# Kernel optimization log

Measured on AMD Instinct MI355X. Metric: run time of the kernel, lower is better.

Reference implementation:

```python
import jax, jax.numpy as jnp
import numpy as np

B, D_TCF, T, GAF_DIM, DK, HIDDEN, N_CLASSES = 128, 512, 1024, 256, 32, 64, 4
EPS = 1e-5

def _glorot(key, shape):
    fan_out, fan_in = shape
    lim = float(np.sqrt(6.0 / (fan_in + fan_out)))
    return jax.random.uniform(key, shape, jnp.float32, -lim, lim)

def setup_inputs() -> dict:
    key = jax.random.key(0)
    ks = jax.random.split(key, 8)
    return {
        "tcf_feat": jax.random.normal(ks[0], (B, D_TCF, T), jnp.float32),
        "gaf_emb": jax.random.normal(ks[1], (B, GAF_DIM), jnp.float32),
        "Wq": _glorot(ks[2], (DK, D_TCF)),        # q_proj.weight [out,in]
        "Wkv": _glorot(ks[3], (DK, GAF_DIM)),     # kv_proj.weight
        "Wout": _glorot(ks[4], (D_TCF, DK)),      # out_proj.weight
        "ln1_g": jnp.ones((D_TCF,), jnp.float32),
        "ln1_b": jnp.zeros((D_TCF,), jnp.float32),
        "W1": _glorot(ks[5], (HIDDEN, D_TCF)),
        "b1": jnp.zeros((HIDDEN,), jnp.float32),
        "ln2_g": jnp.ones((HIDDEN,), jnp.float32),
        "ln2_b": jnp.zeros((HIDDEN,), jnp.float32),
        "W2": _glorot(ks[6], (N_CLASSES, HIDDEN)),
        "b2": jnp.zeros((N_CLASSES,), jnp.float32),
    }

def _layernorm(x, g, b):
    mu = jnp.mean(x, axis=-1, keepdims=True)
    var = jnp.mean(jnp.square(x - mu), axis=-1, keepdims=True)
    return (x - mu) * jax.lax.rsqrt(var + EPS) * g + b

def reference(tcf_feat, gaf_emb, Wq, Wkv, Wout, ln1_g, ln1_b, W1, b1, ln2_g, ln2_b, W2, b2):
    scale = DK ** (-0.5)
    x = jnp.swapaxes(tcf_feat, 1, 2)                      # [B,T,d_tcf]
    Q = jnp.einsum('btd,kd->btk', x, Wq)                  # [B,T,dk]
    KV = gaf_emb @ Wkv.T                                  # [B,dk] (single key/value)
    scores = jnp.einsum('btk,bk->bt', Q, KV) * scale      # [B,T]
    w = jax.nn.softmax(scores, axis=1)                    # softmax over T (dim=1)
    attn_out = w[:, :, None] * KV[:, None, :]             # [B,T,dk]
    y = _layernorm(x + jnp.einsum('btk,dk->btd', attn_out, Wout), ln1_g, ln1_b)
    pooled = jnp.mean(y, axis=1)                          # [B,d_tcf]
    h = jax.nn.elu(_layernorm(pooled @ W1.T + b1, ln2_g, ln2_b))
    return h @ W2.T + b2                                  # [B,n_classes]
```

## Files before the change

kernel.cpp:

```cpp
#include <hip/hip_runtime.h>

#define BN 128
#define DTCF 512
#define TT 1024
#define GAF 256
#define DKK 32
#define HID 64
#define NCLS 4
#define LNEPS 1e-5f
#define DC 8
#define DCL (DTCF/DC)

__global__ __launch_bounds__(256) void k_prep(
    const float* __restrict__ gaf, const float* __restrict__ Wq,
    const float* __restrict__ Wkv, const float* __restrict__ Wout,
    const float* __restrict__ W1,
    float* __restrict__ u, float* __restrict__ qv,
    float* __restrict__ muu, float* __restrict__ varu,
    float* __restrict__ W1t)
{
    int b = blockIdx.x, tid = threadIdx.x;

    if (b >= BN) {
        int e0 = (b - BN) * 4096 + tid * 16;
        int j  = e0 >> 9;
        int dd = e0 & 511;
        #pragma unroll
        for (int i = 0; i < 16; ++i)
            W1t[(dd + i) * HID + j] = W1[j * DTCF + dd + i];
        return;
    }

    __shared__ float gaf_s[GAF];
    __shared__ float kvp[DKK][9];
    __shared__ float kv_s[DKK];
    __shared__ float red[16];

    gaf_s[tid & (GAF - 1)] = gaf[b * GAF + (tid & (GAF - 1))];
    __syncthreads();

    {
        int k = tid >> 3, p8 = tid & 7;
        float acc = 0.f;
        #pragma unroll
        for (int g = p8 * 32; g < p8 * 32 + 32; ++g)
            acc += gaf_s[g] * Wkv[k * GAF + g];
        kvp[k][p8] = acc;
    }
    __syncthreads();
    if (tid < DKK) {
        float a = 0.f;
        #pragma unroll
        for (int p = 0; p < 8; ++p) a += kvp[tid][p];
        kv_s[tid] = a;
    }
    __syncthreads();

    float su = 0.f, suu = 0.f;
    for (int d = tid; d < DTCF; d += 256) {
        float uu = 0.f, qq = 0.f;
        #pragma unroll
        for (int k = 0; k < DKK; ++k) {
            float kv = kv_s[k];
            uu += kv * Wout[d * DKK + k];
            qq += kv * Wq[k * DTCF + d];
        }
        u[b * DTCF + d] = uu;
        qv[b * DTCF + d] = qq;
        su += uu; suu += uu * uu;
    }
    int lane = tid & 63, wv = tid >> 6;
    for (int off = 32; off > 0; off >>= 1) {
        su  += __shfl_down(su, off);
        suu += __shfl_down(suu, off);
    }
    if (lane == 0) { red[wv] = su; red[8 + wv] = suu; }
    __syncthreads();
    if (tid == 0) {
        float s  = red[0] + red[1] + red[2] + red[3];
        float ss = red[8] + red[9] + red[10] + red[11];
        float m = s * (1.f / DTCF);
        muu[b]  = m;
        varu[b] = ss * (1.f / DTCF) - m * m;
    }
}

__global__ __launch_bounds__(256) void k_passA(
    const float* __restrict__ tcf, const float* __restrict__ u,
    const float* __restrict__ qv, float* __restrict__ part)
{
    int b = blockIdx.x, dc = blockIdx.y, tid = threadIdx.x;
    __shared__ float u_s[DCL], qv_s[DCL];
    if (tid < DCL) u_s[tid] = u[b * DTCF + dc * DCL + tid];
    else if (tid < 2 * DCL) qv_s[tid - DCL] = qv[b * DTCF + dc * DCL + (tid - DCL)];
    __syncthreads();

    int t0 = tid * 4;
    const float* base = tcf + ((size_t)b * DTCF + dc * DCL) * TT + t0;
    float4 sx = {0,0,0,0}, sxx = {0,0,0,0}, sxu = {0,0,0,0}, sxq = {0,0,0,0};
    #pragma unroll 4
    for (int d = 0; d < DCL; ++d) {
        float4 v = *(const float4*)(base + (size_t)d * TT);
        float uu = u_s[d], qq = qv_s[d];
        sx.x += v.x; sx.y += v.y; sx.z += v.z; sx.w += v.w;
        sxx.x += v.x*v.x; sxx.y += v.y*v.y; sxx.z += v.z*v.z; sxx.w += v.w*v.w;
        sxu.x += v.x*uu; sxu.y += v.y*uu; sxu.z += v.z*uu; sxu.w += v.w*uu;
        sxq.x += v.x*qq; sxq.y += v.y*qq; sxq.z += v.z*qq; sxq.w += v.w*qq;
    }
    float* p = part + (((size_t)b * DC + dc) * 4) * TT + t0;
    *(float4*)(p)          = sx;
    *(float4*)(p + TT)     = sxx;
    *(float4*)(p + 2 * TT) = sxu;
    *(float4*)(p + 3 * TT) = sxq;
}

__global__ __launch_bounds__(256) void k_soft(
    const float* __restrict__ part, const float* __restrict__ muu,
    const float* __restrict__ varu,
    float* __restrict__ r_o, float* __restrict__ S2, float* __restrict__ S3)
{
    int b = blockIdx.x, tid = threadIdx.x;
    int lane = tid & 63, wv = tid >> 6;
    __shared__ float red[16];
    int t0 = tid * 4;

    float4 sx = {0,0,0,0}, sxx = {0,0,0,0}, sxu = {0,0,0,0}, sxq = {0,0,0,0};
    #pragma unroll
    for (int dc = 0; dc < DC; ++dc) {
        const float* p = part + (((size_t)b * DC + dc) * 4) * TT + t0;
        float4 a = *(const float4*)(p);
        float4 bq = *(const float4*)(p + TT);
        float4 c = *(const float4*)(p + 2 * TT);
        float4 dq = *(const float4*)(p + 3 * TT);
        sx.x += a.x; sx.y += a.y; sx.z += a.z; sx.w += a.w;
        sxx.x += bq.x; sxx.y += bq.y; sxx.z += bq.z; sxx.w += bq.w;
        sxu.x += c.x; sxu.y += c.y; sxu.z += c.z; sxu.w += c.w;
        sxq.x += dq.x; sxq.y += dq.y; sxq.z += dq.z; sxq.w += dq.w;
    }
    float mu = muu[b], vu = varu[b];
    const float inv_d = 1.f / DTCF, scale = 0.17677669529663687f;
    float mx[4], vx[4], cv[4], sc[4];
    float sxa[4] = {sx.x, sx.y, sx.z, sx.w};
    float sxxa[4] = {sxx.x, sxx.y, sxx.z, sxx.w};
    float sxua[4] = {sxu.x, sxu.y, sxu.z, sxu.w};
    float sxqa[4] = {sxq.x, sxq.y, sxq.z, sxq.w};
    #pragma unroll
    for (int i = 0; i < 4; ++i) {
        mx[i] = sxa[i] * inv_d;
        vx[i] = sxxa[i] * inv_d - mx[i] * mx[i];
        cv[i] = sxua[i] * inv_d - mx[i] * mu;
        sc[i] = sxqa[i] * scale;
    }

    float m = fmaxf(fmaxf(sc[0], sc[1]), fmaxf(sc[2], sc[3]));
    for (int off = 32; off > 0; off >>= 1) m = fmaxf(m, __shfl_xor(m, off));
    if (lane == 0) red[wv] = m;
    __syncthreads();
    m = fmaxf(fmaxf(red[0], red[1]), fmaxf(red[2], red[3]));

    float e[4], sum = 0.f;
    #pragma unroll
    for (int i = 0; i < 4; ++i) { e[i] = __expf(sc[i] - m); sum += e[i]; }
    for (int off = 32; off > 0; off >>= 1) sum += __shfl_xor(sum, off);
    if (lane == 0) red[4 + wv] = sum;
    __syncthreads();
    sum = red[4] + red[5] + red[6] + red[7];
    float inv = 1.f / sum;

    float rr4[4], s2a = 0.f, s3a = 0.f;
    #pragma unroll
    for (int i = 0; i < 4; ++i) {
        float w = e[i] * inv;
        float vr = vx[i] + 2.f * w * cv[i] + w * w * vu;
        float rr = rsqrtf(vr + LNEPS);
        rr4[i] = rr;
        s2a += rr * w;
        s3a += rr * mx[i];
    }
    *(float4*)(r_o + (size_t)b * TT + t0) = make_float4(rr4[0], rr4[1], rr4[2], rr4[3]);

    for (int off = 32; off > 0; off >>= 1) {
        s2a += __shfl_xor(s2a, off);
        s3a += __shfl_xor(s3a, off);
    }
    if (lane == 0) { red[8 + wv] = s2a; red[12 + wv] = s3a; }
    __syncthreads();
    if (tid == 0) {
        S2[b] = (red[8] + red[9] + red[10] + red[11]) * (1.f / TT);
        S3[b] = (red[12] + red[13] + red[14] + red[15]) * (1.f / TT);
    }
}

__global__ __launch_bounds__(256) void k_passB(
    const float* __restrict__ tcf, const float* __restrict__ r,
    const float* __restrict__ u, const float* __restrict__ muu,
    const float* __restrict__ S2, const float* __restrict__ S3,
    const float* __restrict__ g1, const float* __restrict__ be1,
    float* __restrict__ pooled)
{
    int b = blockIdx.x, dblk = blockIdx.y;
    int tid = threadIdx.x, wv = tid >> 6, lane = tid & 63;
    int d = dblk * 4 + wv;

    const float* row = tcf + ((size_t)b * DTCF + d) * TT;
    const float* rb  = r + (size_t)b * TT;

    float acc = 0.f;
    #pragma unroll
    for (int i = 0; i < 4; ++i) {
        float4 x = *(const float4*)(row + i * 256 + lane * 4);
        float4 rv = *(const float4*)(rb + i * 256 + lane * 4);
        acc += rv.x * x.x + rv.y * x.y + rv.z * x.z + rv.w * x.w;
    }
    for (int off = 32; off > 0; off >>= 1) acc += __shfl_down(acc, off);

    if (lane == 0) {
        float pd = acc * (1.f / TT) - S3[b] + (u[b * DTCF + d] - muu[b]) * S2[b];
        pooled[b * DTCF + d] = g1[d] * pd + be1[d];
    }
}

__global__ __launch_bounds__(256) void k_head(
    const float* __restrict__ pooled, const float* __restrict__ W1t,
    const float* __restrict__ b1, const float* __restrict__ g2,
    const float* __restrict__ be2, const float* __restrict__ W2,
    const float* __restrict__ b2o, float* __restrict__ out)
{
    int b = blockIdx.x, tid = threadIdx.x;
    int j = tid & 63, wv = tid >> 6;
    __shared__ float p_s[DTCF];
    __shared__ float hred[4][HID];
    for (int i = tid; i < DTCF; i += 256) p_s[i] = pooled[b * DTCF + i];
    __syncthreads();

    float hp = 0.f;
    #pragma unroll 8
    for (int i = 0; i < 128; ++i) {
        int dd = wv * 128 + i;
        hp += p_s[dd] * W1t[dd * HID + j];
    }
    hred[wv][j] = hp;
    __syncthreads();

    if (wv == 0) {
        float h = hred[0][j] + hred[1][j] + hred[2][j] + hred[3][j] + b1[j];
        float mu = h;
        for (int off = 32; off > 0; off >>= 1) mu += __shfl_xor(mu, off);
        mu *= (1.f / HID);
        float df = h - mu;
        float vr = df * df;
        for (int off = 32; off > 0; off >>= 1) vr += __shfl_xor(vr, off);
        vr *= (1.f / HID);
        float hn = df * rsqrtf(vr + LNEPS) * g2[j] + be2[j];
        float he = hn > 0.f ? hn : expm1f(hn);

        #pragma unroll
        for (int c = 0; c < NCLS; ++c) {
            float v = he * W2[c * HID + j];
            for (int off = 32; off > 0; off >>= 1) v += __shfl_xor(v, off);
            if (j == 0) out[b * NCLS + c] = v + b2o[c];
        }
    }
}

extern "C" void kernel_launch(void* const* d_in, const int* in_sizes, int n_in,
                              void* d_out, int out_size, void* d_ws, size_t ws_size,
                              hipStream_t stream)
{
    const float* tcf  = (const float*)d_in[0];
    const float* gaf  = (const float*)d_in[1];
    const float* Wq   = (const float*)d_in[2];
    const float* Wkv  = (const float*)d_in[3];
    const float* Wout = (const float*)d_in[4];
    const float* ln1g = (const float*)d_in[5];
    const float* ln1b = (const float*)d_in[6];
    const float* W1   = (const float*)d_in[7];
    const float* b1   = (const float*)d_in[8];
    const float* ln2g = (const float*)d_in[9];
    const float* ln2b = (const float*)d_in[10];
    const float* W2   = (const float*)d_in[11];
    const float* b2   = (const float*)d_in[12];

    float* ws     = (float*)d_ws;
    float* u      = ws;
    float* qv     = u + BN * DTCF;
    float* muu    = qv + BN * DTCF;
    float* varu   = muu + BN;
    float* r      = varu + BN;
    float* S2     = r + BN * TT;
    float* S3     = S2 + BN;
    float* pooled = S3 + BN;
    float* W1t    = pooled + BN * DTCF;
    float* part   = W1t + DTCF * HID;

    k_prep<<<BN + 8, 256, 0, stream>>>(gaf, Wq, Wkv, Wout, W1, u, qv, muu, varu, W1t);
    k_passA<<<dim3(BN, DC), 256, 0, stream>>>(tcf, u, qv, part);
    k_soft<<<BN, 256, 0, stream>>>(part, muu, varu, r, S2, S3);
    k_passB<<<dim3(BN, DTCF / 4), 256, 0, stream>>>(tcf, r, u, muu, S2, S3, ln1g, ln1b, pooled);
    k_head<<<BN, 256, 0, stream>>>(pooled, W1t, b1, ln2g, ln2b, W2, b2, (float*)d_out);
}
```

Measured before the change: 444.4 us.

## Fuse prep, stats pass and softmax into one 1024-thread kernel per batch

Merges k_prep, k_passA and k_soft into one kernel. Each 1024-thread block handles one batch row: it computes u/qv in shared memory, then every thread scans one time column across all 512 features and does the softmax and rsqrt locally. This removes the partial-sum round trip and two launches. The cost is only 136 blocks of 1024 threads, which may underfill the GPU, and each thread makes 512 strided scalar loads. PassB now walks features in reverse order, so the rows passA touched last are read first while they may still be in cache, and it loads tcf with nontemporal loads.

```diff
diff --git a/kernel.cpp b/kernel.cpp
--- a/kernel.cpp
+++ b/kernel.cpp
@@ -8,44 +8,49 @@
 #define HID 64
 #define NCLS 4
 #define LNEPS 1e-5f
-#define DC 8
-#define DCL (DTCF/DC)
-
-__global__ __launch_bounds__(256) void k_prep(
-    const float* __restrict__ gaf, const float* __restrict__ Wq,
-    const float* __restrict__ Wkv, const float* __restrict__ Wout,
-    const float* __restrict__ W1,
-    float* __restrict__ u, float* __restrict__ qv,
-    float* __restrict__ muu, float* __restrict__ varu,
+#define SCALE 0.17677669529663687f
+
+typedef float f4v __attribute__((ext_vector_type(4)));
+
+__global__ __launch_bounds__(1024, 4) void k_fusedA(
+    const float* __restrict__ tcf, const float* __restrict__ gaf,
+    const float* __restrict__ Wq, const float* __restrict__ Wkv,
+    const float* __restrict__ Wout, const float* __restrict__ W1,
+    float* __restrict__ u, float* __restrict__ muu,
+    float* __restrict__ r_o, float* __restrict__ S2, float* __restrict__ S3,
     float* __restrict__ W1t)
 {
     int b = blockIdx.x, tid = threadIdx.x;
 
     if (b >= BN) {
-        int e0 = (b - BN) * 4096 + tid * 16;
+        int e0 = (b - BN) * 4096 + tid * 4;
         int j  = e0 >> 9;
         int dd = e0 & 511;
         #pragma unroll
-        for (int i = 0; i < 16; ++i)
+        for (int i = 0; i < 4; ++i)
             W1t[(dd + i) * HID + j] = W1[j * DTCF + dd + i];
         return;
     }
 
     __shared__ float gaf_s[GAF];
-    __shared__ float kvp[DKK][9];
+    __shared__ float kvp[DKK][8];
     __shared__ float kv_s[DKK];
-    __shared__ float red[16];
-
-    gaf_s[tid & (GAF - 1)] = gaf[b * GAF + (tid & (GAF - 1))];
-    __syncthreads();
-
-    {
-        int k = tid >> 3, p8 = tid & 7;
-        float acc = 0.f;
+    __shared__ float2 uq_s[DTCF];
+    __shared__ float red[32];
+    __shared__ float stats[2];
+
+    int lane = tid & 63, wv = tid >> 6;
+
+    if (tid < GAF) gaf_s[tid] = gaf[b * GAF + tid];
+    __syncthreads();
+
+    if ((tid & 31) < 8) {
+        int k = tid >> 5, p8 = tid & 7;
+        float a = 0.f;
         #pragma unroll
         for (int g = p8 * 32; g < p8 * 32 + 32; ++g)
-            acc += gaf_s[g] * Wkv[k * GAF + g];
-        kvp[k][p8] = acc;
+            a += gaf_s[g] * Wkv[k * GAF + g];
+        kvp[k][p8] = a;
     }
     __syncthreads();
     if (tid < DKK) {
@@ -56,138 +61,98 @@
     }
     __syncthreads();
 
-    float su = 0.f, suu = 0.f;
-    for (int d = tid; d < DTCF; d += 256) {
-        float uu = 0.f, qq = 0.f;
-        #pragma unroll
-        for (int k = 0; k < DKK; ++k) {
-            float kv = kv_s[k];
-            uu += kv * Wout[d * DKK + k];
-            qq += kv * Wq[k * DTCF + d];
+    if (tid < DTCF) {
+        int d = tid;
+        float uu = 0.f;
+        #pragma unroll
+        for (int k = 0; k < DKK; ++k) uu += kv_s[k] * Wout[d * DKK + k];
+        uq_s[d].x = uu;
+        u[b * DTCF + d] = uu;
+        float su = uu, suu = uu * uu;
+        #pragma unroll
+        for (int off = 32; off > 0; off >>= 1) {
+            su  += __shfl_down(su, off);
+            suu += __shfl_down(suu, off);
         }
-        u[b * DTCF + d] = uu;
-        qv[b * DTCF + d] = qq;
-        su += uu; suu += uu * uu;
-    }
-    int lane = tid & 63, wv = tid >> 6;
-    for (int off = 32; off > 0; off >>= 1) {
-        su  += __shfl_down(su, off);
-        suu += __shfl_down(suu, off);
-    }
-    if (lane == 0) { red[wv] = su; red[8 + wv] = suu; }
+        if (lane == 0) { red[wv] = su; red[16 + wv] = suu; }
+    } else {
+        int d = tid - DTCF;
+        float qq = 0.f;
+        #pragma unroll
+        for (int k = 0; k < DKK; ++k) qq += kv_s[k] * Wq[k * DTCF + d];
+        uq_s[d].y = qq;
+    }
     __syncthreads();
     if (tid == 0) {
-        float s  = red[0] + red[1] + red[2] + red[3];
-        float ss = red[8] + red[9] + red[10] + red[11];
+        float s = 0.f, ss = 0.f;
+        #pragma unroll
+        for (int i = 0; i < 8; ++i) { s += red[i]; ss += red[16 + i]; }
         float m = s * (1.f / DTCF);
-        muu[b]  = m;
-        varu[b] = ss * (1.f / DTCF) - m * m;
-    }
-}
-
-__global__ __launch_bounds__(256) void k_passA(
-    const float* __restrict__ tcf, const float* __restrict__ u,
-    const float* __restrict__ qv, float* __restrict__ part)
-{
-    int b = blockIdx.x, dc = blockIdx.y, tid = threadIdx.x;
-    __shared__ float u_s[DCL], qv_s[DCL];
-    if (tid < DCL) u_s[tid] = u[b * DTCF + dc * DCL + tid];
-    else if (tid < 2 * DCL) qv_s[tid - DCL] = qv[b * DTCF + dc * DCL + (tid - DCL)];
-    __syncthreads();
-
-    int t0 = tid * 4;
-    const float* base = tcf + ((size_t)b * DTCF + dc * DCL) * TT + t0;
-    float4 sx = {0,0,0,0}, sxx = {0,0,0,0}, sxu = {0,0,0,0}, sxq = {0,0,0,0};
-    #pragma unroll 4
-    for (int d = 0; d < DCL; ++d) {
-        float4 v = *(const float4*)(base + (size_t)d * TT);
-        float uu = u_s[d], qq = qv_s[d];
-        sx.x += v.x; sx.y += v.y; sx.z += v.z; sx.w += v.w;
-        sxx.x += v.x*v.x; sxx.y += v.y*v.y; sxx.z += v.z*v.z; sxx.w += v.w*v.w;
-        sxu.x += v.x*uu; sxu.y += v.y*uu; sxu.z += v.z*uu; sxu.w += v.w*uu;
-        sxq.x += v.x*qq; sxq.y += v.y*qq; sxq.z += v.z*qq; sxq.w += v.w*qq;
-    }
-    float* p = part + (((size_t)b * DC + dc) * 4) * TT + t0;
-    *(float4*)(p)          = sx;
-    *(float4*)(p + TT)     = sxx;
-    *(float4*)(p + 2 * TT) = sxu;
-    *(float4*)(p + 3 * TT) = sxq;
-}
-
-__global__ __launch_bounds__(256) void k_soft(
-    const float* __restrict__ part, const float* __restrict__ muu,
-    const float* __restrict__ varu,
-    float* __restrict__ r_o, float* __restrict__ S2, float* __restrict__ S3)
-{
-    int b = blockIdx.x, tid = threadIdx.x;
-    int lane = tid & 63, wv = tid >> 6;
-    __shared__ float red[16];
-    int t0 = tid * 4;
-
-    float4 sx = {0,0,0,0}, sxx = {0,0,0,0}, sxu = {0,0,0,0}, sxq = {0,0,0,0};
-    #pragma unroll
-    for (int dc = 0; dc < DC; ++dc) {
-        const float* p = part + (((size_t)b * DC + dc) * 4) * TT + t0;
-        float4 a = *(const float4*)(p);
-        float4 bq = *(const float4*)(p + TT);
-        float4 c = *(const float4*)(p + 2 * TT);
-        float4 dq = *(const float4*)(p + 3 * TT);
-        sx.x += a.x; sx.y += a.y; sx.z += a.z; sx.w += a.w;
-        sxx.x += bq.x; sxx.y += bq.y; sxx.z += bq.z; sxx.w += bq.w;
-        sxu.x += c.x; sxu.y += c.y; sxu.z += c.z; sxu.w += c.w;
-        sxq.x += dq.x; sxq.y += dq.y; sxq.z += dq.z; sxq.w += dq.w;
-    }
-    float mu = muu[b], vu = varu[b];
-    const float inv_d = 1.f / DTCF, scale = 0.17677669529663687f;
-    float mx[4], vx[4], cv[4], sc[4];
-    float sxa[4] = {sx.x, sx.y, sx.z, sx.w};
-    float sxxa[4] = {sxx.x, sxx.y, sxx.z, sxx.w};
-    float sxua[4] = {sxu.x, sxu.y, sxu.z, sxu.w};
-    float sxqa[4] = {sxq.x, sxq.y, sxq.z, sxq.w};
-    #pragma unroll
-    for (int i = 0; i < 4; ++i) {
-        mx[i] = sxa[i] * inv_d;
-        vx[i] = sxxa[i] * inv_d - mx[i] * mx[i];
-        cv[i] = sxua[i] * inv_d - mx[i] * mu;
-        sc[i] = sxqa[i] * scale;
-    }
-
-    float m = fmaxf(fmaxf(sc[0], sc[1]), fmaxf(sc[2], sc[3]));
+        stats[0] = m;
+        stats[1] = ss * (1.f / DTCF) - m * m;
+        muu[b] = m;
+    }
+    __syncthreads();
+    float mu_u = stats[0], var_u = stats[1];
+
+    const float* col = tcf + (size_t)b * (DTCF * TT) + tid;
+    float sx = 0.f, sxx = 0.f, sxu = 0.f, sxq = 0.f;
+    #pragma unroll 16
+    for (int d = 0; d < DTCF; ++d) {
+        float v = col[d << 10];
+        float2 uq = uq_s[d];
+        sx  += v;
+        sxx += v * v;
+        sxu += v * uq.x;
+        sxq += v * uq.y;
+    }
+
+    const float inv_d = 1.f / DTCF;
+    float mx = sx * inv_d;
+    float vx = sxx * inv_d - mx * mx;
+    float cv = sxu * inv_d - mx * mu_u;
+    float sc = sxq * SCALE;
+
+    float m = sc;
+    #pragma unroll
     for (int off = 32; off > 0; off >>= 1) m = fmaxf(m, __shfl_xor(m, off));
     if (lane == 0) red[wv] = m;
     __syncthreads();
-    m = fmaxf(fmaxf(red[0], red[1]), fmaxf(red[2], red[3]));
-
-    float e[4], sum = 0.f;
-    #pragma unroll
-    for (int i = 0; i < 4; ++i) { e[i] = __expf(sc[i] - m); sum += e[i]; }
-    for (int off = 32; off > 0; off >>= 1) sum += __shfl_xor(sum, off);
-    if (lane == 0) red[4 + wv] = sum;
-    __syncthreads();
-    sum = red[4] + red[5] + red[6] + red[7];
-    float inv = 1.f / sum;
-
-    float rr4[4], s2a = 0.f, s3a = 0.f;
-    #pragma unroll
-    for (int i = 0; i < 4; ++i) {
-        float w = e[i] * inv;
-        float vr = vx[i] + 2.f * w * cv[i] + w * w * vu;
-        float rr = rsqrtf(vr + LNEPS);
-        rr4[i] = rr;
-        s2a += rr * w;
-        s3a += rr * mx[i];
-    }
-    *(float4*)(r_o + (size_t)b * TT + t0) = make_float4(rr4[0], rr4[1], rr4[2], rr4[3]);
-
+    m = red[0];
+    #pragma unroll
+    for (int i = 1; i < 16; ++i) m = fmaxf(m, red[i]);
+
+    float e = __expf(sc - m);
+    float s = e;
+    #pragma unroll
+    for (int off = 32; off > 0; off >>= 1) s += __shfl_xor(s, off);
+    if (lane == 0) red[16 + wv] = s;
+    __syncthreads();
+    s = 0.f;
+    #pragma unroll
+    for (int i = 0; i < 16; ++i) s += red[16 + i];
+    float inv = 1.f / s;
+
+    float w  = e * inv;
+    float vr = vx + 2.f * w * cv + w * w * var_u;
+    float rr = rsqrtf(vr + LNEPS);
+    r_o[b * TT + tid] = rr;
+
+    float s2p = rr * w, s3p = rr * mx;
+    #pragma unroll
     for (int off = 32; off > 0; off >>= 1) {
-        s2a += __shfl_xor(s2a, off);
-        s3a += __shfl_xor(s3a, off);
-    }
-    if (lane == 0) { red[8 + wv] = s2a; red[12 + wv] = s3a; }
+        s2p += __shfl_xor(s2p, off);
+        s3p += __shfl_xor(s3p, off);
+    }
+    __syncthreads();
+    if (lane == 0) { red[wv] = s2p; red[16 + wv] = s3p; }
     __syncthreads();
     if (tid == 0) {
-        S2[b] = (red[8] + red[9] + red[10] + red[11]) * (1.f / TT);
-        S3[b] = (red[12] + red[13] + red[14] + red[15]) * (1.f / TT);
+        float a2 = 0.f, a3 = 0.f;
+        #pragma unroll
+        for (int i = 0; i < 16; ++i) { a2 += red[i]; a3 += red[16 + i]; }
+        S2[b] = a2 * (1.f / TT);
+        S3[b] = a3 * (1.f / TT);
     }
 }
 
@@ -198,9 +163,9 @@
     const float* __restrict__ g1, const float* __restrict__ be1,
     float* __restrict__ pooled)
 {
-    int b = blockIdx.x, dblk = blockIdx.y;
+    int b = blockIdx.x, yb = blockIdx.y;
     int tid = threadIdx.x, wv = tid >> 6, lane = tid & 63;
-    int d = dblk * 4 + wv;
+    int d = (DTCF - 4) - yb * 4 + wv;
 
     const float* row = tcf + ((size_t)b * DTCF + d) * TT;
     const float* rb  = r + (size_t)b * TT;
@@ -208,7 +173,7 @@
     float acc = 0.f;
     #pragma unroll
     for (int i = 0; i < 4; ++i) {
-        float4 x = *(const float4*)(row + i * 256 + lane * 4);
+        f4v    x  = __builtin_nontemporal_load((const f4v*)(row + i * 256 + lane * 4));
         float4 rv = *(const float4*)(rb + i * 256 + lane * 4);
         acc += rv.x * x.x + rv.y * x.y + rv.z * x.z + rv.w * x.w;
     }
@@ -283,19 +248,17 @@
 
     float* ws     = (float*)d_ws;
     float* u      = ws;
-    float* qv     = u + BN * DTCF;
-    float* muu    = qv + BN * DTCF;
-    float* varu   = muu + BN;
-    float* r      = varu + BN;
+    float* muu    = u + BN * DTCF;
+    float* r      = muu + BN;
     float* S2     = r + BN * TT;
     float* S3     = S2 + BN;
     float* pooled = S3 + BN;
     float* W1t    = pooled + BN * DTCF;
-    float* part   = W1t + DTCF * HID;
-
-    k_prep<<<BN + 8, 256, 0, stream>>>(gaf, Wq, Wkv, Wout, W1, u, qv, muu, varu, W1t);
-    k_passA<<<dim3(BN, DC), 256, 0, stream>>>(tcf, u, qv, part);
-    k_soft<<<BN, 256, 0, stream>>>(part, muu, varu, r, S2, S3);
-    k_passB<<<dim3(BN, DTCF / 4), 256, 0, stream>>>(tcf, r, u, muu, S2, S3, ln1g, ln1b, pooled);
-    k_head<<<BN, 256, 0, stream>>>(pooled, W1t, b1, ln2g, ln2b, W2, b2, (float*)d_out);
-}
+
+    k_fusedA<<<BN + 8, 1024, 0, stream>>>(tcf, gaf, Wq, Wkv, Wout, W1,
+                                          u, muu, r, S2, S3, W1t);
+    k_passB<<<dim3(BN, DTCF / 4), 256, 0, stream>>>(tcf, r, u, muu, S2, S3,
+                                                    ln1g, ln1b, pooled);
+    k_head<<<BN, 256, 0, stream>>>(pooled, W1t, b1, ln2g, ln2b, W2, b2,
+                                   (float*)d_out);
+}
```

After: 424.4 us. 1.05x faster.
